# Optimization experiments

Hardware: AMD Instinct MI355X
Metric: run time of the kernel (lower is better)

## Reference

```python
import jax, jax.numpy as jnp
import numpy as np

N = 50000      # nodes
E = 800000     # edges (before self-loops)
H = 4          # attention heads
C = 32         # out_features per head
DIN = 128      # in_features (== H*C so residual path is active)
ED = 16        # edge_dim
NEG = 0.2      # LeakyReLU negative slope (GATConv default)
EPS = 1e-5     # LayerNorm eps


def setup_inputs() -> dict:
    key = jax.random.key(0)
    ks = jax.random.split(key, 12)
    s = 0.05
    return {
        "x": jax.random.normal(ks[0], (N, DIN), dtype=jnp.float32),
        "edge_index": jax.random.randint(ks[1], (2, E), 0, N, dtype=jnp.int64),
        "edge_attr": jax.random.normal(ks[2], (E, ED), dtype=jnp.float32),
        # edge_processor: Linear(ED, ED) + ReLU (dropout = identity at eval)
        "W_ep": jax.random.normal(ks[3], (ED, ED), dtype=jnp.float32) * s,
        "b_ep": jnp.zeros((ED,), dtype=jnp.float32),
        # GATConv params (lin / lin_edge are bias-free in PyG)
        "W_lin": jax.random.normal(ks[4], (DIN, H * C), dtype=jnp.float32) * s,
        "W_edge": jax.random.normal(ks[5], (ED, H * C), dtype=jnp.float32) * s,
        "att_src": jax.random.normal(ks[6], (H, C), dtype=jnp.float32) * s,
        "att_dst": jax.random.normal(ks[7], (H, C), dtype=jnp.float32) * s,
        "att_edge": jax.random.normal(ks[8], (H, C), dtype=jnp.float32) * s,
        "bias": jnp.zeros((H * C,), dtype=jnp.float32),
        # LayerNorm params
        "ln_g": jnp.ones((H * C,), dtype=jnp.float32),
        "ln_b": jnp.zeros((H * C,), dtype=jnp.float32),
    }


def reference(x, edge_index, edge_attr, W_ep, b_ep, W_lin, W_edge,
              att_src, att_dst, att_edge, bias, ln_g, ln_b):
    n = x.shape[0]
    src, dst = edge_index[0], edge_index[1]

    # edge_processor: Linear + ReLU
    ea = jax.nn.relu(edge_attr @ W_ep + b_ep)                       # [E, ED]

    # add self-loops (PyG GATConv default), loop edge_attr = mean of incoming
    ones = jnp.ones((ea.shape[0],), dtype=ea.dtype)
    deg = jax.ops.segment_sum(ones, dst, num_segments=n)            # [N]
    loop_attr = jax.ops.segment_sum(ea, dst, num_segments=n)
    loop_attr = loop_attr / jnp.maximum(deg, 1.0)[:, None]          # [N, ED]
    loop = jnp.arange(n, dtype=src.dtype)
    src2 = jnp.concatenate([src, loop])                             # [E+N]
    dst2 = jnp.concatenate([dst, loop])
    ea2 = jnp.concatenate([ea, loop_attr], axis=0)                  # [E+N, ED]

    # node / edge linear transforms
    h = (x @ W_lin).reshape(n, H, C)                                # [N, H, C]
    a_src = jnp.einsum('nhc,hc->nh', h, att_src)                    # [N, H]
    a_dst = jnp.einsum('nhc,hc->nh', h, att_dst)
    e = (ea2 @ W_edge).reshape(-1, H, C)                            # [E+N, H, C]
    a_e = jnp.einsum('ehc,hc->eh', e, att_edge)                     # [E+N, H]

    # per-edge attention logits + leaky relu
    alpha = a_src[src2] + a_dst[dst2] + a_e                         # [E+N, H]
    alpha = jnp.where(alpha >= 0, alpha, NEG * alpha)

    # segment softmax over incoming edges of each dst node
    m = jax.ops.segment_max(alpha, dst2, num_segments=n)            # [N, H]
    ex = jnp.exp(alpha - m[dst2])
    denom = jax.ops.segment_sum(ex, dst2, num_segments=n)           # [N, H]
    w = ex / denom[dst2]                                            # [E+N, H]

    # scatter-aggregate messages
    msg = h[src2] * w[:, :, None]                                   # [E+N, H, C]
    out = jax.ops.segment_sum(msg, dst2, num_segments=n)            # [N, H, C]
    out = out.reshape(n, H * C) + bias

    # residual (DIN == H*C) + LayerNorm
    out = out + x
    mu = jnp.mean(out, axis=-1, keepdims=True)
    var = jnp.var(out, axis=-1, keepdims=True)
    out = (out - mu) * jax.lax.rsqrt(var + EPS) * ln_g + ln_b
    return out
```

## Files before the change

### kernel.cpp

```cpp
#include <hip/hip_runtime.h>
#include <hip/hip_fp16.h>
#include <math.h>

#define NN   50000
#define EE   800000
#define HH   4
#define CC   32
#define DINN 128
#define ED   16
#define NEGS 0.2f
#define LNEPS 1e-5f
#define CPAD 32
#define SLOT 64

struct __align__(16) Hp4 { __half2 a, b, c, d; };

__global__ __launch_bounds__(256, 3) void k_node(
        const float* __restrict__ x, const float* __restrict__ W_lin,
        const float* __restrict__ att_src, const float* __restrict__ att_dst,
        __half* __restrict__ hb, float* __restrict__ a_src, float* __restrict__ a_dst) {
    __shared__ float xr[64 * 132];
    int t = threadIdx.x;
    int row0 = blockIdx.x * 64;

    #pragma unroll
    for (int i = 0; i < 8; ++i) {
        int idx = t + 256 * i;
        int r = idx >> 5, kq = idx & 31;
        int row = row0 + r;
        float4 v = make_float4(0.f, 0.f, 0.f, 0.f);
        if (row < NN) v = ((const float4*)x)[(long)row * 32 + kq];
        *(float4*)&xr[r * 132 + kq * 4] = v;
    }
    __syncthreads();

    int colg = t & 15, rowg = t >> 4;
    int c0 = colg * 8;
    const float* Wp = W_lin + c0;
    float acc[4][8] = {};

    #pragma unroll 2
    for (int k = 0; k < DINN; k += 2) {
        float4 wa0 = *(const float4*)&Wp[(long)k * DINN];
        float4 wb0 = *(const float4*)&Wp[(long)k * DINN + 4];
        float4 wa1 = *(const float4*)&Wp[(long)(k + 1) * DINN];
        float4 wb1 = *(const float4*)&Wp[(long)(k + 1) * DINN + 4];
        #pragma unroll
        for (int i = 0; i < 4; ++i) {
            float2 xv = *(const float2*)&xr[(rowg * 4 + i) * 132 + k];
            acc[i][0] = fmaf(xv.x, wa0.x, acc[i][0]);
            acc[i][1] = fmaf(xv.x, wa0.y, acc[i][1]);
            acc[i][2] = fmaf(xv.x, wa0.z, acc[i][2]);
            acc[i][3] = fmaf(xv.x, wa0.w, acc[i][3]);
            acc[i][4] = fmaf(xv.x, wb0.x, acc[i][4]);
            acc[i][5] = fmaf(xv.x, wb0.y, acc[i][5]);
            acc[i][6] = fmaf(xv.x, wb0.z, acc[i][6]);
            acc[i][7] = fmaf(xv.x, wb0.w, acc[i][7]);
            acc[i][0] = fmaf(xv.y, wa1.x, acc[i][0]);
            acc[i][1] = fmaf(xv.y, wa1.y, acc[i][1]);
            acc[i][2] = fmaf(xv.y, wa1.z, acc[i][2]);
            acc[i][3] = fmaf(xv.y, wa1.w, acc[i][3]);
            acc[i][4] = fmaf(xv.y, wb1.x, acc[i][4]);
            acc[i][5] = fmaf(xv.y, wb1.y, acc[i][5]);
            acc[i][6] = fmaf(xv.y, wb1.z, acc[i][6]);
            acc[i][7] = fmaf(xv.y, wb1.w, acc[i][7]);
        }
    }

    int head = colg >> 2;
    int cw = c0 & 31;
    float4 as0 = *(const float4*)&att_src[head * CC + cw];
    float4 as1 = *(const float4*)&att_src[head * CC + cw + 4];
    float4 ad0 = *(const float4*)&att_dst[head * CC + cw];
    float4 ad1 = *(const float4*)&att_dst[head * CC + cw + 4];
    #pragma unroll
    for (int i = 0; i < 4; ++i) {
        int row = row0 + rowg * 4 + i;
        if (row < NN) {
            Hp4 p;
            p.a = __floats2half2_rn(acc[i][0], acc[i][1]);
            p.b = __floats2half2_rn(acc[i][2], acc[i][3]);
            p.c = __floats2half2_rn(acc[i][4], acc[i][5]);
            p.d = __floats2half2_rn(acc[i][6], acc[i][7]);
            *(Hp4*)&hb[(long)row * DINN + c0] = p;
        }
        float ps = acc[i][0]*as0.x + acc[i][1]*as0.y + acc[i][2]*as0.z + acc[i][3]*as0.w
                 + acc[i][4]*as1.x + acc[i][5]*as1.y + acc[i][6]*as1.z + acc[i][7]*as1.w;
        float pd = acc[i][0]*ad0.x + acc[i][1]*ad0.y + acc[i][2]*ad0.z + acc[i][3]*ad0.w
                 + acc[i][4]*ad1.x + acc[i][5]*ad1.y + acc[i][6]*ad1.z + acc[i][7]*ad1.w;
        ps += __shfl_xor(ps, 1); ps += __shfl_xor(ps, 2);
        pd += __shfl_xor(pd, 1); pd += __shfl_xor(pd, 2);
        if ((colg & 3) == 0 && row < NN) {
            a_src[row * 4 + head] = ps;
            a_dst[row * 4 + head] = pd;
        }
    }
}

__device__ __forceinline__ void edge_compute(
        const float a[ED], const float* __restrict__ Wl,
        const float* __restrict__ bl, const float* __restrict__ vl,
        float4 s4, float4 d4, int src, int dst, int rk,
        uint4* __restrict__ pk, int* __restrict__ bsrc) {
    float r[ED];
    #pragma unroll
    for (int j = 0; j < ED; ++j) r[j] = bl[j];
    #pragma unroll
    for (int d = 0; d < ED; ++d) {
        float av = a[d];
        #pragma unroll
        for (int j = 0; j < ED; ++j) r[j] = fmaf(av, Wl[d * ED + j], r[j]);
    }

    float ae0 = 0.f, ae1 = 0.f, ae2 = 0.f, ae3 = 0.f;
    #pragma unroll
    for (int d = 0; d < ED; ++d) {
        float rd = fmaxf(r[d], 0.f);
        ae0 = fmaf(rd, vl[d * 4 + 0], ae0);
        ae1 = fmaf(rd, vl[d * 4 + 1], ae1);
        ae2 = fmaf(rd, vl[d * 4 + 2], ae2);
        ae3 = fmaf(rd, vl[d * 4 + 3], ae3);
    }

    float v0 = s4.x + d4.x + ae0;
    float v1 = s4.y + d4.y + ae1;
    float v2 = s4.z + d4.z + ae2;
    float v3 = s4.w + d4.w + ae3;
    v0 = (v0 >= 0.f) ? v0 : NEGS * v0;
    v1 = (v1 >= 0.f) ? v1 : NEGS * v1;
    v2 = (v2 >= 0.f) ? v2 : NEGS * v2;
    v3 = (v3 >= 0.f) ? v3 : NEGS * v3;

    __half2 p0 = __floats2half2_rn(__expf(v0), ae0);
    __half2 p1 = __floats2half2_rn(__expf(v1), ae1);
    __half2 p2 = __floats2half2_rn(__expf(v2), ae2);
    __half2 p3 = __floats2half2_rn(__expf(v3), ae3);
    if (rk < SLOT) {
        long q = (long)dst * SLOT + rk;
        pk[q] = make_uint4(*(unsigned*)&p0, *(unsigned*)&p1,
                           *(unsigned*)&p2, *(unsigned*)&p3);
        bsrc[q] = src;
    }
}

__global__ __launch_bounds__(256) void k_edgeA(
        const int* __restrict__ ei, const float* __restrict__ edge_attr,
        const float* __restrict__ W_ep, const float* __restrict__ b_ep,
        const float* __restrict__ W_edge, const float* __restrict__ att_edge,
        const float* __restrict__ a_src, const float* __restrict__ a_dst,
        int* __restrict__ cnt, uint4* __restrict__ pk, int* __restrict__ bsrc) {
    __shared__ float Wl[ED * ED];
    __shared__ float bl[ED];
    __shared__ float vl[ED * 4];
    int t = threadIdx.x;
    if (t < ED * ED) Wl[t] = W_ep[t];
    if (t < ED) bl[t] = b_ep[t];
    if (t >= 192 && t < 192 + 64) {
        int q = t - 192;
        int d = q >> 2, h = q & 3;
        float s = 0.f;
        #pragma unroll 8
        for (int c = 0; c < CC; ++c)
            s += W_edge[d * (HH * CC) + h * CC + c] * att_edge[h * CC + c];
        vl[q] = s;
    }
    __syncthreads();

    int e0 = blockIdx.x * 512 + t;
    int e1 = e0 + 256;

    if ((blockIdx.x + 1) * 512 <= EE) {
        int s0 = ei[e0], s1 = ei[e1];
        int d0 = ei[EE + e0], d1 = ei[EE + e1];

        const float4* ap0 = (const float4*)(edge_attr + (long)e0 * ED);
        const float4* ap1 = (const float4*)(edge_attr + (long)e1 * ED);
        float4 A0 = ap0[0], A1 = ap0[1], A2 = ap0[2], A3 = ap0[3];
        float4 B0 = ap1[0], B1 = ap1[1], B2 = ap1[2], B3 = ap1[3];

        int rk0 = atomicAdd(cnt + (long)d0 * CPAD, 1);
        int rk1 = atomicAdd(cnt + (long)d1 * CPAD, 1);

        float4 sa = *(const float4*)&a_src[s0 * 4];
        float4 sb = *(const float4*)&a_src[s1 * 4];
        float4 da = *(const float4*)&a_dst[d0 * 4];
        float4 db = *(const float4*)&a_dst[d1 * 4];

        float a0[ED];
        a0[0]=A0.x; a0[1]=A0.y; a0[2]=A0.z; a0[3]=A0.w;
        a0[4]=A1.x; a0[5]=A1.y; a0[6]=A1.z; a0[7]=A1.w;
        a0[8]=A2.x; a0[9]=A2.y; a0[10]=A2.z; a0[11]=A2.w;
        a0[12]=A3.x; a0[13]=A3.y; a0[14]=A3.z; a0[15]=A3.w;
        edge_compute(a0, Wl, bl, vl, sa, da, s0, d0, rk0, pk, bsrc);

        float a1[ED];
        a1[0]=B0.x; a1[1]=B0.y; a1[2]=B0.z; a1[3]=B0.w;
        a1[4]=B1.x; a1[5]=B1.y; a1[6]=B1.z; a1[7]=B1.w;
        a1[8]=B2.x; a1[9]=B2.y; a1[10]=B2.z; a1[11]=B2.w;
        a1[12]=B3.x; a1[13]=B3.y; a1[14]=B3.z; a1[15]=B3.w;
        edge_compute(a1, Wl, bl, vl, sb, db, s1, d1, rk1, pk, bsrc);
    } else {
        #pragma unroll
        for (int u = 0; u < 2; ++u) {
            int e = e0 + u * 256;
            if (e >= EE) break;
            int src = ei[e];
            int dst = ei[EE + e];
            const float4* ap = (const float4*)(edge_attr + (long)e * ED);
            float4 A0 = ap[0], A1 = ap[1], A2 = ap[2], A3 = ap[3];
            int rk = atomicAdd(cnt + (long)dst * CPAD, 1);
            float4 s4 = *(const float4*)&a_src[src * 4];
            float4 d4 = *(const float4*)&a_dst[dst * 4];
            float a[ED];
            a[0]=A0.x; a[1]=A0.y; a[2]=A0.z; a[3]=A0.w;
            a[4]=A1.x; a[5]=A1.y; a[6]=A1.z; a[7]=A1.w;
            a[8]=A2.x; a[9]=A2.y; a[10]=A2.z; a[11]=A2.w;
            a[12]=A3.x; a[13]=A3.y; a[14]=A3.z; a[15]=A3.w;
            edge_compute(a, Wl, bl, vl, s4, d4, src, dst, rk, pk, bsrc);
        }
    }
}

__global__ __launch_bounds__(256) void k_aggregate(
        const float* __restrict__ x, const __half2* __restrict__ hb,
        const float* __restrict__ a_src, const float* __restrict__ a_dst,
        const int* __restrict__ cnt,
        const unsigned* __restrict__ pkh, const int* __restrict__ srcs,
        const float* __restrict__ bias, const float* __restrict__ ln_g,
        const float* __restrict__ ln_b, float* __restrict__ out) {
    int t = threadIdx.x;
    int wave = t >> 6, lane = t & 63;
    int n = blockIdx.x * 4 + wave;
    if (n >= NN) return;

    int deg = cnt[(long)n * CPAD];
    if (deg > SLOT) deg = SLOT;
    long start = (long)n * SLOT;
    int head = lane >> 4;

    float accx = 0.f, accy = 0.f, s_own = 0.f, aes_own = 0.f;
    const unsigned* pp = pkh + (size_t)start * 4 + head;
    const int* sp = srcs + start;

    int k = 0;
    for (; k + 8 <= deg; k += 8) {
        unsigned pv[8]; int sv[8];
        #pragma unroll
        for (int j = 0; j < 8; ++j) {
            pv[j] = pp[(size_t)(k + j) * 4];
            sv[j] = sp[k + j];
        }
        __half2 hv[8];
        #pragma unroll
        for (int j = 0; j < 8; ++j) hv[j] = hb[(long)sv[j] * 64 + lane];
        #pragma unroll
        for (int j = 0; j < 8; ++j) {
            float2 wf = __half22float2(*(__half2*)&pv[j]);
            s_own += wf.x;
            aes_own += wf.y;
            float2 hf = __half22float2(hv[j]);
            accx = fmaf(wf.x, hf.x, accx);
            accy = fmaf(wf.x, hf.y, accy);
        }
    }
    for (; k < deg; ++k) {
        unsigned p = pp[(size_t)k * 4];
        int src = sp[k];
        __half2 hv = hb[(long)src * 64 + lane];
        float2 wf = __half22float2(*(__half2*)&p);
        s_own += wf.x;
        aes_own += wf.y;
        float2 hf = __half22float2(hv);
        accx = fmaf(wf.x, hf.x, accx);
        accy = fmaf(wf.x, hf.y, accy);
    }

    float inv_deg = 1.0f / fmaxf((float)deg, 1.0f);
    float v = a_src[n * 4 + head] + a_dst[n * 4 + head] + aes_own * inv_deg;
    v = (v >= 0.f) ? v : NEGS * v;
    float w0 = __expf(v);
    s_own += w0;
    float2 hn = __half22float2(hb[(long)n * 64 + lane]);
    accx = fmaf(w0, hn.x, accx);
    accy = fmaf(w0, hn.y, accy);
    float is = 1.0f / s_own;
    accx *= is; accy *= is;

    int c0 = lane * 2;
    float2 b2 = *(const float2*)&bias[c0];
    float2 x2 = *(const float2*)&x[(long)n * DINN + c0];
    float oa = accx + b2.x + x2.x;
    float ob = accy + b2.y + x2.y;
    float sum = oa + ob, sumsq = oa * oa + ob * ob;
    #pragma unroll
    for (int d2 = 1; d2 < 64; d2 <<= 1) {
        sum   += __shfl_xor(sum, d2);
        sumsq += __shfl_xor(sumsq, d2);
    }
    float mu  = sum * (1.0f / DINN);
    float var = sumsq * (1.0f / DINN) - mu * mu;
    float rs  = rsqrtf(var + LNEPS);
    float2 g2  = *(const float2*)&ln_g[c0];
    float2 lb2 = *(const float2*)&ln_b[c0];
    float2 o2;
    o2.x = (oa - mu) * rs * g2.x + lb2.x;
    o2.y = (ob - mu) * rs * g2.y + lb2.y;
    *(float2*)&out[(long)n * DINN + c0] = o2;
}

extern "C" void kernel_launch(void* const* d_in, const int* in_sizes, int n_in,
                              void* d_out, int out_size, void* d_ws, size_t ws_size,
                              hipStream_t stream) {
    const float* x         = (const float*)d_in[0];
    const int*   ei        = (const int*)d_in[1];
    const float* edge_attr = (const float*)d_in[2];
    const float* W_ep      = (const float*)d_in[3];
    const float* b_ep      = (const float*)d_in[4];
    const float* W_lin     = (const float*)d_in[5];
    const float* W_edge    = (const float*)d_in[6];
    const float* att_src   = (const float*)d_in[7];
    const float* att_dst   = (const float*)d_in[8];
    const float* att_edge  = (const float*)d_in[9];
    const float* bias      = (const float*)d_in[10];
    const float* ln_g      = (const float*)d_in[11];
    const float* ln_b      = (const float*)d_in[12];
    float* out = (float*)d_out;

    char* ws = (char*)d_ws;
    size_t o = 0;
    auto take = [&](size_t bytes) -> char* {
        char* p = ws + o;
        o = (o + bytes + 255) & ~(size_t)255;
        return p;
    };
    __half* hbuf  = (__half*)take((size_t)NN * DINN * 2);
    float*  a_src = (float*)take((size_t)NN * 4 * 4);
    float*  a_dst = (float*)take((size_t)NN * 4 * 4);
    int*    cnt   = (int*)  take((size_t)NN * CPAD * 4);
    uint4*  pk    = (uint4*)take((size_t)NN * SLOT * 16);
    int*    bsrc  = (int*)  take((size_t)NN * SLOT * 4);

    hipMemsetAsync(cnt, 0, (size_t)NN * CPAD * 4, stream);

    k_node<<<(NN + 63) / 64, 256, 0, stream>>>(x, W_lin, att_src, att_dst,
                                               hbuf, a_src, a_dst);
    k_edgeA<<<(EE + 511) / 512, 256, 0, stream>>>(ei, edge_attr, W_ep, b_ep,
                                                  W_edge, att_edge, a_src, a_dst,
                                                  cnt, pk, bsrc);
    k_aggregate<<<(NN + 3) / 4, 256, 0, stream>>>(x, (const __half2*)hbuf,
                                                  a_src, a_dst, cnt,
                                                  (const unsigned*)pk, bsrc,
                                                  bias, ln_g, ln_b, out);
}
```

Measured before the change: 276.6 us.

## Move attention exp into aggregate, pack src into record, fold cnt memset into node kernel

```diff
diff --git a/kernel.cpp b/kernel.cpp
--- a/kernel.cpp
+++ b/kernel.cpp
@@ -18,10 +18,17 @@
 __global__ __launch_bounds__(256, 3) void k_node(
         const float* __restrict__ x, const float* __restrict__ W_lin,
         const float* __restrict__ att_src, const float* __restrict__ att_dst,
-        __half* __restrict__ hb, float* __restrict__ a_src, float* __restrict__ a_dst) {
+        __half* __restrict__ hb, float* __restrict__ a_src, float* __restrict__ a_dst,
+        int* __restrict__ cnt) {
     __shared__ float xr[64 * 132];
     int t = threadIdx.x;
     int row0 = blockIdx.x * 64;
+
+    #pragma unroll
+    for (int i = 0; i < 8; ++i) {
+        int idx = blockIdx.x * 2048 + i * 256 + t;
+        if (idx < NN * CPAD) cnt[idx] = 0;
+    }
 
     #pragma unroll
     for (int i = 0; i < 8; ++i) {
@@ -98,10 +105,16 @@
 }
 
 __device__ __forceinline__ void edge_compute(
-        const float a[ED], const float* __restrict__ Wl,
-        const float* __restrict__ bl, const float* __restrict__ vl,
-        float4 s4, float4 d4, int src, int dst, int rk,
-        uint4* __restrict__ pk, int* __restrict__ bsrc) {
+        float4 A0, float4 A1, float4 A2, float4 A3,
+        const float* __restrict__ Wl, const float* __restrict__ bl,
+        const float* __restrict__ vl,
+        int src, int dst, int rk, uint4* __restrict__ pk) {
+    float a[ED];
+    a[0]=A0.x; a[1]=A0.y; a[2]=A0.z; a[3]=A0.w;
+    a[4]=A1.x; a[5]=A1.y; a[6]=A1.z; a[7]=A1.w;
+    a[8]=A2.x; a[9]=A2.y; a[10]=A2.z; a[11]=A2.w;
+    a[12]=A3.x; a[13]=A3.y; a[14]=A3.z; a[15]=A3.w;
+
     float r[ED];
     #pragma unroll
     for (int j = 0; j < ED; ++j) r[j] = bl[j];
@@ -122,24 +135,12 @@
         ae3 = fmaf(rd, vl[d * 4 + 3], ae3);
     }
 
-    float v0 = s4.x + d4.x + ae0;
-    float v1 = s4.y + d4.y + ae1;
-    float v2 = s4.z + d4.z + ae2;
-    float v3 = s4.w + d4.w + ae3;
-    v0 = (v0 >= 0.f) ? v0 : NEGS * v0;
-    v1 = (v1 >= 0.f) ? v1 : NEGS * v1;
-    v2 = (v2 >= 0.f) ? v2 : NEGS * v2;
-    v3 = (v3 >= 0.f) ? v3 : NEGS * v3;
-
-    __half2 p0 = __floats2half2_rn(__expf(v0), ae0);
-    __half2 p1 = __floats2half2_rn(__expf(v1), ae1);
-    __half2 p2 = __floats2half2_rn(__expf(v2), ae2);
-    __half2 p3 = __floats2half2_rn(__expf(v3), ae3);
+    __half2 ae01 = __floats2half2_rn(ae0, ae1);
+    __half2 ae23 = __floats2half2_rn(ae2, ae3);
     if (rk < SLOT) {
         long q = (long)dst * SLOT + rk;
-        pk[q] = make_uint4(*(unsigned*)&p0, *(unsigned*)&p1,
-                           *(unsigned*)&p2, *(unsigned*)&p3);
-        bsrc[q] = src;
+        pk[q] = make_uint4(*(unsigned*)&ae01, *(unsigned*)&ae23,
+                           (unsigned)src, 0u);
     }
 }
 
@@ -147,8 +148,7 @@
         const int* __restrict__ ei, const float* __restrict__ edge_attr,
         const float* __restrict__ W_ep, const float* __restrict__ b_ep,
         const float* __restrict__ W_edge, const float* __restrict__ att_edge,
-        const float* __restrict__ a_src, const float* __restrict__ a_dst,
-        int* __restrict__ cnt, uint4* __restrict__ pk, int* __restrict__ bsrc) {
+        int* __restrict__ cnt, uint4* __restrict__ pk) {
     __shared__ float Wl[ED * ED];
     __shared__ float bl[ED];
     __shared__ float vl[ED * 4];
@@ -181,24 +181,8 @@
         int rk0 = atomicAdd(cnt + (long)d0 * CPAD, 1);
         int rk1 = atomicAdd(cnt + (long)d1 * CPAD, 1);
 
-        float4 sa = *(const float4*)&a_src[s0 * 4];
-        float4 sb = *(const float4*)&a_src[s1 * 4];
-        float4 da = *(const float4*)&a_dst[d0 * 4];
-        float4 db = *(const float4*)&a_dst[d1 * 4];
-
-        float a0[ED];
-        a0[0]=A0.x; a0[1]=A0.y; a0[2]=A0.z; a0[3]=A0.w;
-        a0[4]=A1.x; a0[5]=A1.y; a0[6]=A1.z; a0[7]=A1.w;
-        a0[8]=A2.x; a0[9]=A2.y; a0[10]=A2.z; a0[11]=A2.w;
-        a0[12]=A3.x; a0[13]=A3.y; a0[14]=A3.z; a0[15]=A3.w;
-        edge_compute(a0, Wl, bl, vl, sa, da, s0, d0, rk0, pk, bsrc);
-
-        float a1[ED];
-        a1[0]=B0.x; a1[1]=B0.y; a1[2]=B0.z; a1[3]=B0.w;
-        a1[4]=B1.x; a1[5]=B1.y; a1[6]=B1.z; a1[7]=B1.w;
-        a1[8]=B2.x; a1[9]=B2.y; a1[10]=B2.z; a1[11]=B2.w;
-        a1[12]=B3.x; a1[13]=B3.y; a1[14]=B3.z; a1[15]=B3.w;
-        edge_compute(a1, Wl, bl, vl, sb, db, s1, d1, rk1, pk, bsrc);
+        edge_compute(A0, A1, A2, A3, Wl, bl, vl, s0, d0, rk0, pk);
+        edge_compute(B0, B1, B2, B3, Wl, bl, vl, s1, d1, rk1, pk);
     } else {
         #pragma unroll
         for (int u = 0; u < 2; ++u) {
@@ -209,14 +193,7 @@
             const float4* ap = (const float4*)(edge_attr + (long)e * ED);
             float4 A0 = ap[0], A1 = ap[1], A2 = ap[2], A3 = ap[3];
             int rk = atomicAdd(cnt + (long)dst * CPAD, 1);
-            float4 s4 = *(const float4*)&a_src[src * 4];
-            float4 d4 = *(const float4*)&a_dst[dst * 4];
-            float a[ED];
-            a[0]=A0.x; a[1]=A0.y; a[2]=A0.z; a[3]=A0.w;
-            a[4]=A1.x; a[5]=A1.y; a[6]=A1.z; a[7]=A1.w;
-            a[8]=A2.x; a[9]=A2.y; a[10]=A2.z; a[11]=A2.w;
-            a[12]=A3.x; a[13]=A3.y; a[14]=A3.z; a[15]=A3.w;
-            edge_compute(a, Wl, bl, vl, s4, d4, src, dst, rk, pk, bsrc);
+            edge_compute(A0, A1, A2, A3, Wl, bl, vl, src, dst, rk, pk);
         }
     }
 }
@@ -224,8 +201,7 @@
 __global__ __launch_bounds__(256) void k_aggregate(
         const float* __restrict__ x, const __half2* __restrict__ hb,
         const float* __restrict__ a_src, const float* __restrict__ a_dst,
-        const int* __restrict__ cnt,
-        const unsigned* __restrict__ pkh, const int* __restrict__ srcs,
+        const int* __restrict__ cnt, const uint4* __restrict__ pk,
         const float* __restrict__ bias, const float* __restrict__ ln_g,
         const float* __restrict__ ln_b, float* __restrict__ out) {
     int t = threadIdx.x;
@@ -235,48 +211,61 @@
 
     int deg = cnt[(long)n * CPAD];
     if (deg > SLOT) deg = SLOT;
-    long start = (long)n * SLOT;
+    const uint4* rp = pk + (long)n * SLOT;
     int head = lane >> 4;
 
+    float adn = a_dst[n * 4 + head];
     float accx = 0.f, accy = 0.f, s_own = 0.f, aes_own = 0.f;
-    const unsigned* pp = pkh + (size_t)start * 4 + head;
-    const int* sp = srcs + start;
 
     int k = 0;
     for (; k + 8 <= deg; k += 8) {
-        unsigned pv[8]; int sv[8];
+        uint4 rv[8];
+        #pragma unroll
+        for (int j = 0; j < 8; ++j) rv[j] = rp[k + j];
+        __half2 hv[8];
+        float asv[8];
         #pragma unroll
         for (int j = 0; j < 8; ++j) {
-            pv[j] = pp[(size_t)(k + j) * 4];
-            sv[j] = sp[k + j];
-        }
-        __half2 hv[8];
-        #pragma unroll
-        for (int j = 0; j < 8; ++j) hv[j] = hb[(long)sv[j] * 64 + lane];
+            int src = (int)rv[j].z;
+            hv[j] = hb[(long)src * 64 + lane];
+            asv[j] = a_src[src * 4 + head];
+        }
         #pragma unroll
         for (int j = 0; j < 8; ++j) {
-            float2 wf = __half22float2(*(__half2*)&pv[j]);
-            s_own += wf.x;
-            aes_own += wf.y;
+            unsigned aw = (head & 2) ? rv[j].y : rv[j].x;
+            float2 aef = __half22float2(*(__half2*)&aw);
+            float ae = (head & 1) ? aef.y : aef.x;
+            float v = asv[j] + adn + ae;
+            v = (v >= 0.f) ? v : NEGS * v;
+            float w = __expf(v);
+            s_own += w;
+            aes_own += ae;
             float2 hf = __half22float2(hv[j]);
-            accx = fmaf(wf.x, hf.x, accx);
-            accy = fmaf(wf.x, hf.y, accy);
+            accx = fmaf(w, hf.x, accx);
+            accy = fmaf(w, hf.y, accy);
         }
     }
     for (; k < deg; ++k) {
-        unsigned p = pp[(size_t)k * 4];
-        int src = sp[k];
+        uint4 rv = rp[k];
+        int src = (int)rv.z;
         __half2 hv = hb[(long)src * 64 + lane];
-        float2 wf = __half22float2(*(__half2*)&p);
-        s_own += wf.x;
-        aes_own += wf.y;
+        float as = a_src[src * 4 + head];
+        unsigned aw = (head & 2) ? rv.y : rv.x;
+        float2 aef = __half22float2(*(__half2*)&aw);
+        float ae = (head & 1) ? aef.y : aef.x;
+        float v = as + adn + ae;
+        v = (v >= 0.f) ? v : NEGS * v;
+        float w = __expf(v);
+        s_own += w;
+        aes_own += ae;
         float2 hf = __half22float2(hv);
-        accx = fmaf(wf.x, hf.x, accx);
-        accy = fmaf(wf.x, hf.y, accy);
-    }
-
+        accx = fmaf(w, hf.x, accx);
+        accy = fmaf(w, hf.y, accy);
+    }
+
+    float asn = a_src[n * 4 + head];
     float inv_deg = 1.0f / fmaxf((float)deg, 1.0f);
-    float v = a_src[n * 4 + head] + a_dst[n * 4 + head] + aes_own * inv_deg;
+    float v = asn + adn + aes_own * inv_deg;
     v = (v >= 0.f) ? v : NEGS * v;
     float w0 = __expf(v);
     s_own += w0;
@@ -338,17 +327,13 @@
     float*  a_dst = (float*)take((size_t)NN * 4 * 4);
     int*    cnt   = (int*)  take((size_t)NN * CPAD * 4);
     uint4*  pk    = (uint4*)take((size_t)NN * SLOT * 16);
-    int*    bsrc  = (int*)  take((size_t)NN * SLOT * 4);
-
-    hipMemsetAsync(cnt, 0, (size_t)NN * CPAD * 4, stream);
 
     k_node<<<(NN + 63) / 64, 256, 0, stream>>>(x, W_lin, att_src, att_dst,
-                                               hbuf, a_src, a_dst);
+                                               hbuf, a_src, a_dst, cnt);
     k_edgeA<<<(EE + 511) / 512, 256, 0, stream>>>(ei, edge_attr, W_ep, b_ep,
-                                                  W_edge, att_edge, a_src, a_dst,
-                                                  cnt, pk, bsrc);
+                                                  W_edge, att_edge, cnt, pk);
     k_aggregate<<<(NN + 3) / 4, 256, 0, stream>>>(x, (const __half2*)hbuf,
                                                   a_src, a_dst, cnt,
-                                                  (const unsigned*)pk, bsrc,
+                                                  (const uint4*)pk,
                                                   bias, ln_g, ln_b, out);
 }
```

Result: slower. 383.1 us (+38.5%).
